# Optimization experiments

Hardware: AMD Instinct MI355X
Metric: run time of the kernel (lower is better)

## Reference

```python
import jax, jax.numpy as jnp
import numpy as np

N_ENT = 100000   # n_entities
N_REL = 64       # n_relations
E_DIM = 64       # e_dim == r_dim (rel2ent is None)
K = 32           # neighbors per entity
B = 1024         # batch of seed entities
SLOPE = 0.2      # LeakyReLU negative_slope


def _xavier(key, shape, fan_in, fan_out):
    b = (6.0 / (fan_in + fan_out)) ** 0.5
    return jax.random.uniform(key, shape, jnp.float32, -b, b)


def setup_inputs() -> dict:
    key = jax.random.key(0)
    ks = jax.random.split(key, 10)
    E = _xavier(ks[0], (N_ENT, E_DIM), N_ENT, E_DIM)          # entity_embs.weight
    R = _xavier(ks[1], (N_REL, E_DIM), N_REL, E_DIM)          # relation_embs.weight
    att_w1 = _xavier(ks[2], (E_DIM, 2 * E_DIM), 2 * E_DIM, E_DIM)  # attention[0], no bias
    att_w2 = _xavier(ks[3], (E_DIM, E_DIM), E_DIM, E_DIM)          # attention[2], no bias
    att_w3 = _xavier(ks[4], (1, E_DIM), E_DIM, 1)                  # attention[4], no bias
    wx_w = _xavier(ks[5], (E_DIM, E_DIM), E_DIM, E_DIM)            # Wx[0].weight
    wx_b = jnp.zeros((E_DIM,), jnp.float32)                        # Wx[0].bias
    wc_w = _xavier(ks[6], (E_DIM, 2 * E_DIM), 2 * E_DIM, E_DIM)    # W_concat.weight
    wc_b = jnp.zeros((E_DIM,), jnp.float32)                        # W_concat.bias
    entity_idx = jax.random.randint(ks[7], (B,), 0, N_ENT)
    adj_entity = jax.random.randint(ks[8], (N_ENT, K), 0, N_ENT)
    adj_relation = jax.random.randint(ks[9], (N_ENT, K), 0, N_REL)
    return {
        "entity_idx": entity_idx, "adj_entity": adj_entity, "adj_relation": adj_relation,
        "E": E, "R": R, "att_w1": att_w1, "att_w2": att_w2, "att_w3": att_w3,
        "wx_w": wx_w, "wx_b": wx_b, "wc_w": wc_w, "wc_b": wc_b,
    }


def _lookup(W, idx):
    # nn.Embedding(max_norm=1): rows whose L2 norm exceeds 1 are renormalized.
    e = W[idx]
    n = jnp.linalg.norm(e, axis=-1, keepdims=True)
    return e * jnp.where(n > 1.0, 1.0 / (n + 1e-7), 1.0)


def _forward(entity_idx, adj_entity, adj_relation, E, R,
             att_w1, att_w2, att_w3, wx_w, wx_b, wc_w, wc_b):
    leaky = lambda x: jnp.where(x >= 0, x, SLOPE * x)
    # attention MLP on cat([h, r]): split first linear so the broadcast h term
    # is computed once per batch row instead of materializing [B, N, 2e].
    w1h, w1r = att_w1[:, :E_DIM], att_w1[:, E_DIM:]

    def gat(h, r, t):
        # h: [B, e] (broadcast over neighbors), r,t: [B, N, e]
        hid = jax.nn.relu(jnp.einsum('be,fe->bf', h, w1h)[:, None, :]
                          + jnp.einsum('bne,fe->bnf', r, w1r))
        hid = jax.nn.relu(jnp.einsum('bnf,gf->bng', hid, att_w2))
        a = jax.nn.sigmoid(jnp.einsum('bng,og->bno', hid, att_w3)[..., 0])  # [B, N]
        w = jax.nn.softmax(a, axis=-1)
        agg = jnp.einsum('bn,bne->be', w, t)       # softmax-weighted neighbor sum
        return agg @ wx_w.T + wx_b                 # per-head Linear (n_heads=1)

    Bsz = entity_idx.shape[0]
    # hop-1 / hop-2 neighbor index gathers (get_neighbors)
    ent1 = adj_entity[entity_idx]                  # [B, K]
    rel1 = adj_relation[entity_idx]                # [B, K]
    ent2 = adj_entity[ent1].reshape(Bsz, -1)       # [B, K*K]
    rel2 = adj_relation[ent1].reshape(Bsz, -1)     # [B, K*K]

    h = _lookup(E, entity_idx)                     # [B, e]
    t1 = _lookup(E, ent1)                          # [B, K, e]
    t2 = _lookup(E, ent2)                          # [B, K*K, e]
    r1 = _lookup(R, rel1)
    r2 = _lookup(R, rel2)

    # iter 0: seed entity broadcast as head
    v1 = leaky(gat(h, r1, t1))                                      # [B, e]
    emb1 = leaky(jnp.concatenate([h, v1], -1) @ wc_w.T + wc_b)      # aggregate 'concat'
    # iter 1: summed hop-1 neighborhood as head
    hsum = t1.sum(axis=1)                                           # [B, e]
    v2 = leaky(gat(hsum, r2, t2))
    emb2 = leaky(jnp.concatenate([hsum, v2], -1) @ wc_w.T + wc_b)
    # sum_aggregator 'concat': e_u = cat(embs[2], cat(embs[1], embs[0]))
    return jnp.concatenate([emb2, emb1, h], axis=-1)                # [B, 3e]


def reference(entity_idx, adj_entity, adj_relation, E, R,
              att_w1, att_w2, att_w3, wx_w, wx_b, wc_w, wc_b):
    return _forward(entity_idx, adj_entity, adj_relation, E, R,
                    att_w1, att_w2, att_w3, wx_w, wx_b, wc_w, wc_b)
```

## Files before the change

kernel.cpp:

```cpp
#include <hip/hip_runtime.h>

#define SLOPE 0.2f

__device__ __forceinline__ float leaky(float x) { return x >= 0.f ? x : SLOPE * x; }

enum : int {
  OFF_PT   = 0,
  OFF_W2T  = OFF_PT + 4096,
  OFF_A3   = OFF_W2T + 4096,
  OFF_WXT  = OFF_A3 + 64,
  OFF_WXB  = OFF_WXT + 4096,
  OFF_WCT  = OFF_WXB + 64,
  OFF_WCB  = OFF_WCT + 8192,
  OFF_W1HT = OFF_WCB + 64,
  WS_FLOATS = OFF_W1HT + 4096
};

__global__ __launch_bounds__(256) void k1_prep(
    const float* __restrict__ R, const float* __restrict__ w1,
    const float* __restrict__ w2, const float* __restrict__ w3,
    const float* __restrict__ wxw, const float* __restrict__ wxb,
    const float* __restrict__ wcw, const float* __restrict__ wcb,
    float* __restrict__ ws) {
  __shared__ float Rn[64 * 65];
  int tid = threadIdx.x, wv = tid >> 6, lane = tid & 63;
  for (int r = wv; r < 64; r += 4) {
    float v = R[r * 64 + lane];
    float ss = v * v;
    #pragma unroll
    for (int m = 1; m < 64; m <<= 1) ss += __shfl_xor(ss, m, 64);
    float n = sqrtf(ss);
    float sc = n > 1.f ? 1.f / (n + 1e-7f) : 1.f;
    Rn[r * 65 + lane] = v * sc;
  }
  __syncthreads();
  int gt = blockIdx.x * 256 + tid;
  for (int i = gt; i < 4096; i += 2048) {
    int f = i >> 6, r = i & 63;
    float acc = 0.f;
    #pragma unroll
    for (int e = 0; e < 64; ++e) acc += Rn[r * 65 + e] * w1[f * 128 + 64 + e];
    ws[OFF_PT + f * 64 + r] = acc;
  }
  for (int i = gt; i < 4096; i += 2048) {
    int f = i >> 6, g = i & 63;
    ws[OFF_W2T + i] = w2[g * 64 + f];
  }
  for (int i = gt; i < 4096; i += 2048) {
    int e = i >> 6, f = i & 63;
    ws[OFF_WXT + i]  = wxw[f * 64 + e];
    ws[OFF_W1HT + i] = w1[f * 128 + e];
  }
  for (int i = gt; i < 8192; i += 2048) {
    int e = i >> 6, f = i & 63;
    ws[OFF_WCT + i] = wcw[f * 128 + e];
  }
  if (gt < 64) {
    ws[OFF_A3 + gt]  = w3[gt];
    ws[OFF_WXB + gt] = wxb[gt];
    ws[OFF_WCB + gt] = wcb[gt];
  }
}

__global__ __launch_bounds__(512, 8) void k_main(
    const int* __restrict__ entity_idx, const int* __restrict__ adj_entity,
    const int* __restrict__ adj_relation, const float* __restrict__ E,
    const float* __restrict__ ws, float* __restrict__ out) {
  __shared__ float s_t1[32 * 64];
  __shared__ float s_partA[8][64], s_partB[8][64];
  __shared__ int   s_ent1[32], s_rel1[32];
  __shared__ int   s_ei[1024];
  __shared__ float s_w[1024];
  __shared__ float s_h[64], s_hs[64], s_hq1[64], s_hq2[64];
  __shared__ float s_at1[64], s_at2[64], s_agg1[64], s_agg2[64], s_v1[64], s_v2[64];
  __shared__ float s_L1, s_L2;
  int b = blockIdx.x, tid = threadIdx.x, wv = tid >> 6, lane = tid & 63;
  int sub = lane >> 4, eg = lane & 15;
  const float4* E4 = (const float4*)E;
  int idx = entity_idx[b];

  if (tid < 64) s_h[tid] = E[(long)idx * 64 + tid];
  if (tid >= 64 && tid < 96) {
    int i = tid - 64;
    s_ent1[i] = adj_entity[(long)idx * 32 + i];
    s_rel1[i] = adj_relation[(long)idx * 32 + i];
  }
  if (tid == 0) s_L2 = 0.f;
  __syncthreads();

  {
    float hs = 0.f;
    #pragma unroll
    for (int k = 0; k < 4; ++k) {
      int n = wv * 4 + k;
      float v = E[(long)s_ent1[n] * 64 + lane];
      s_t1[n * 64 + lane] = v;
      hs += v;
    }
    s_partA[wv][lane] = hs;
  }
  __syncthreads();
  if (tid < 64) {
    float t = 0.f;
    #pragma unroll
    for (int w = 0; w < 8; ++w) t += s_partA[w][tid];
    s_hs[tid] = t;
  }
  __syncthreads();

  {
    const float* src = (wv < 4) ? s_h : s_hs;
    int e0 = (wv & 3) * 16;
    float p = 0.f;
    #pragma unroll
    for (int e = 0; e < 16; ++e) p += ws[OFF_W1HT + (e0 + e) * 64 + lane] * src[e0 + e];
    s_partB[wv][lane] = p;
  }
  __syncthreads();
  if (tid < 64) {
    s_hq1[tid] = s_partB[0][tid] + s_partB[1][tid] + s_partB[2][tid] + s_partB[3][tid];
  } else if (tid < 128) {
    int i = tid - 64;
    s_hq2[i] = s_partB[4][i] + s_partB[5][i] + s_partB[6][i] + s_partB[7][i];
  }
  __syncthreads();

  {
    int swv = __builtin_amdgcn_readfirstlane(wv);
    const float* W2T = ws + OFF_W2T;
    const float* A3  = ws + OFF_A3;
    const float* PT  = ws + OFF_PT;
    float acc1[8], acc2[8];
    #pragma unroll
    for (int i = 0; i < 8; ++i) { acc1[i] = 0.f; acc2[i] = 0.f; }
    int g0 = swv * 8;
    #pragma unroll 2
    for (int f = 0; f < 64; ++f) {
      float ptv = PT[f * 64 + lane];
      float h1 = fmaxf(s_hq1[f] + ptv, 0.f);
      float h2 = fmaxf(s_hq2[f] + ptv, 0.f);
      const float* w = W2T + f * 64 + g0;
      #pragma unroll
      for (int i = 0; i < 8; ++i) { acc1[i] += w[i] * h1; acc2[i] += w[i] * h2; }
    }
    float s1 = 0.f, s2 = 0.f;
    #pragma unroll
    for (int i = 0; i < 8; ++i) {
      float a3 = A3[g0 + i];
      s1 += a3 * fmaxf(acc1[i], 0.f);
      s2 += a3 * fmaxf(acc2[i], 0.f);
    }
    s_partA[wv][lane] = s1;
    s_partB[wv][lane] = s2;
  }
  __syncthreads();
  if (tid < 64) {
    float t = 0.f;
    #pragma unroll
    for (int w = 0; w < 8; ++w) t += s_partA[w][tid];
    float a = 1.f / (1.f + __expf(-t));
    s_at1[tid] = __expf(a);
  } else if (tid < 128) {
    int i = tid - 64;
    float t = 0.f;
    #pragma unroll
    for (int w = 0; w < 8; ++w) t += s_partB[w][i];
    float a = 1.f / (1.f + __expf(-t));
    s_at2[i] = __expf(a);
  }
  __syncthreads();

  {
    float wsum = 0.f;
    #pragma unroll
    for (int i = 0; i < 2; ++i) {
      int n = tid + i * 512;
      int j = n >> 5, i2 = n & 31;
      long base = (long)s_ent1[j] * 32 + i2;
      int ei = adj_entity[base];
      int ri = adj_relation[base];
      float wgt = s_at2[ri];
      s_ei[n] = ei;
      s_w[n] = wgt;
      wsum += wgt;
    }
    #pragma unroll
    for (int m = 1; m < 64; m <<= 1) wsum += __shfl_xor(wsum, m, 64);
    if (lane == 0) atomicAdd(&s_L2, wsum);
  }
  if (tid < 32) {
    float w = s_at1[s_rel1[tid]];
    #pragma unroll
    for (int m = 1; m < 32; m <<= 1) w += __shfl_xor(w, m, 64);
    if (tid == 0) s_L1 = w;
  }
  __syncthreads();

  {
    float4 acc = {0.f, 0.f, 0.f, 0.f};
    for (int t = 0; t < 8; ++t) {
      float4 v[4];
      int nb = t * 4 * 32 + wv * 4 + sub;
      #pragma unroll
      for (int j = 0; j < 4; ++j)
        v[j] = E4[(long)s_ei[nb + j * 32] * 16 + eg];
      #pragma unroll
      for (int j = 0; j < 4; ++j) {
        float wgt = s_w[nb + j * 32];
        acc.x += wgt * v[j].x; acc.y += wgt * v[j].y;
        acc.z += wgt * v[j].z; acc.w += wgt * v[j].w;
      }
    }
    #pragma unroll
    for (int m = 16; m < 64; m <<= 1) {
      acc.x += __shfl_xor(acc.x, m, 64); acc.y += __shfl_xor(acc.y, m, 64);
      acc.z += __shfl_xor(acc.z, m, 64); acc.w += __shfl_xor(acc.w, m, 64);
    }
    if (sub == 0) {
      s_partB[wv][eg * 4 + 0] = acc.x; s_partB[wv][eg * 4 + 1] = acc.y;
      s_partB[wv][eg * 4 + 2] = acc.z; s_partB[wv][eg * 4 + 3] = acc.w;
    }
  }
  {
    float a1 = 0.f;
    #pragma unroll
    for (int k = 0; k < 4; ++k) {
      int n = wv * 4 + k;
      a1 += s_at1[s_rel1[n]] * s_t1[n * 64 + lane];
    }
    s_partA[wv][lane] = a1;
  }
  __syncthreads();
  if (tid < 64) {
    float a = 0.f;
    #pragma unroll
    for (int w = 0; w < 8; ++w) a += s_partA[w][tid];
    s_agg1[tid] = a / s_L1;
  } else if (tid < 128) {
    int i = tid - 64;
    float a = 0.f;
    #pragma unroll
    for (int w = 0; w < 8; ++w) a += s_partB[w][i];
    s_agg2[i] = a / s_L2;
  }
  __syncthreads();

  {
    const float* src = (wv < 4) ? s_agg1 : s_agg2;
    int e0 = (wv & 3) * 16;
    float p = 0.f;
    #pragma unroll
    for (int e = 0; e < 16; ++e)
      p += ws[OFF_WXT + (e0 + e) * 64 + lane] * src[e0 + e];
    s_partA[wv][lane] = p;
  }
  __syncthreads();
  if (tid < 64) {
    float p = s_partA[0][tid] + s_partA[1][tid] + s_partA[2][tid] + s_partA[3][tid];
    s_v1[tid] = leaky(ws[OFF_WXB + tid] + p);
  } else if (tid < 128) {
    int i = tid - 64;
    float p = s_partA[4][i] + s_partA[5][i] + s_partA[6][i] + s_partA[7][i];
    s_v2[i] = leaky(ws[OFF_WXB + i] + p);
  }
  __syncthreads();

  {
    int half = wv >> 2, q = wv & 3;
    const float* src = (q < 2) ? (half ? s_hs : s_h) : (half ? s_v2 : s_v1);
    int e0 = q * 32;
    int o0 = (q & 1) * 32;
    float p = 0.f;
    #pragma unroll 8
    for (int e = 0; e < 32; ++e)
      p += ws[OFF_WCT + (e0 + e) * 64 + lane] * src[o0 + e];
    s_partB[wv][lane] = p;
  }
  __syncthreads();
  if (tid < 64) {
    float o = ws[OFF_WCB + tid] + s_partB[0][tid] + s_partB[1][tid]
            + s_partB[2][tid] + s_partB[3][tid];
    out[b * 192 + 64 + tid]  = leaky(o);
    out[b * 192 + 128 + tid] = s_h[tid];
  } else if (tid < 128) {
    int i = tid - 64;
    float o = ws[OFF_WCB + i] + s_partB[4][i] + s_partB[5][i]
            + s_partB[6][i] + s_partB[7][i];
    out[b * 192 + i] = leaky(o);
  }
}

extern "C" void kernel_launch(void* const* d_in, const int* in_sizes, int n_in,
                              void* d_out, int out_size, void* d_ws, size_t ws_size,
                              hipStream_t stream) {
  const int* entity_idx   = (const int*)d_in[0];
  const int* adj_entity   = (const int*)d_in[1];
  const int* adj_relation = (const int*)d_in[2];
  const float* E          = (const float*)d_in[3];
  const float* R          = (const float*)d_in[4];
  const float* att_w1     = (const float*)d_in[5];
  const float* att_w2     = (const float*)d_in[6];
  const float* att_w3     = (const float*)d_in[7];
  const float* wx_w       = (const float*)d_in[8];
  const float* wx_b       = (const float*)d_in[9];
  const float* wc_w       = (const float*)d_in[10];
  const float* wc_b       = (const float*)d_in[11];
  float* out              = (float*)d_out;
  float* ws               = (float*)d_ws;

  hipLaunchKernelGGL(k1_prep, dim3(8), dim3(256), 0, stream,
                     R, att_w1, att_w2, att_w3, wx_w, wx_b, wc_w, wc_b, ws);
  hipLaunchKernelGGL(k_main, dim3(1024), dim3(512), 0, stream,
                     entity_idx, adj_entity, adj_relation, E, ws, out);
}
```

Measured before the change: 165.8 us.

## Convert entity table to bf16 each call and gather hop-2 rows in bf16

The prep kernel gains 1600 extra blocks that convert the whole 100000x64 fp32 entity table into packed bf16 with round-to-nearest-even and write it to workspace. The hop-2 weighted aggregation then gathers 128-byte bf16 rows as uint4 instead of 256-byte fp32 rows, unpacks them to fp32 and accumulates with a new lane mapping. The aim is to halve the random-gather bytes for the 1024 neighbour rows per seed. The trade is a full-table conversion pass on every call (about 25.6MB read and 12.8MB written) plus reduced precision in that aggregation.

```diff
diff --git a/kernel.cpp b/kernel.cpp
--- a/kernel.cpp
+++ b/kernel.cpp
@@ -13,7 +13,8 @@
   OFF_WCT  = OFF_WXB + 64,
   OFF_WCB  = OFF_WCT + 8192,
   OFF_W1HT = OFF_WCB + 64,
-  WS_FLOATS = OFF_W1HT + 4096
+  WS_FLOATS = OFF_W1HT + 4096,
+  EBF_U32  = 3200000
 };
 
 __global__ __launch_bounds__(256) void k1_prep(
@@ -21,9 +22,24 @@
     const float* __restrict__ w2, const float* __restrict__ w3,
     const float* __restrict__ wxw, const float* __restrict__ wxb,
     const float* __restrict__ wcw, const float* __restrict__ wcb,
-    float* __restrict__ ws) {
+    const float* __restrict__ E, float* __restrict__ ws) {
+  int tid = threadIdx.x;
+  if (blockIdx.x >= 8) {
+    const float2* E2 = (const float2*)E;
+    unsigned* Ebf = (unsigned*)ws + WS_FLOATS;
+    int stride = (gridDim.x - 8) * 256;
+    for (int i = (blockIdx.x - 8) * 256 + tid; i < EBF_U32; i += stride) {
+      float2 f = E2[i];
+      unsigned ua = __float_as_uint(f.x);
+      ua += 0x7FFFu + ((ua >> 16) & 1u);
+      unsigned ub = __float_as_uint(f.y);
+      ub += 0x7FFFu + ((ub >> 16) & 1u);
+      Ebf[i] = (ua >> 16) | (ub & 0xFFFF0000u);
+    }
+    return;
+  }
   __shared__ float Rn[64 * 65];
-  int tid = threadIdx.x, wv = tid >> 6, lane = tid & 63;
+  int wv = tid >> 6, lane = tid & 63;
   for (int r = wv; r < 64; r += 4) {
     float v = R[r * 64 + lane];
     float ss = v * v;
@@ -75,8 +91,8 @@
   __shared__ float s_at1[64], s_at2[64], s_agg1[64], s_agg2[64], s_v1[64], s_v2[64];
   __shared__ float s_L1, s_L2;
   int b = blockIdx.x, tid = threadIdx.x, wv = tid >> 6, lane = tid & 63;
-  int sub = lane >> 4, eg = lane & 15;
   const float4* E4 = (const float4*)E;
+  (void)E4;
   int idx = entity_idx[b];
 
   if (tid < 64) s_h[tid] = E[(long)idx * 64 + tid];
@@ -197,28 +213,41 @@
   __syncthreads();
 
   {
-    float4 acc = {0.f, 0.f, 0.f, 0.f};
-    for (int t = 0; t < 8; ++t) {
-      float4 v[4];
-      int nb = t * 4 * 32 + wv * 4 + sub;
-      #pragma unroll
-      for (int j = 0; j < 4; ++j)
-        v[j] = E4[(long)s_ei[nb + j * 32] * 16 + eg];
+    const uint4* Ebf = (const uint4*)((const unsigned*)ws + WS_FLOATS);
+    int sub8 = lane >> 3, eg8 = lane & 7;
+    float acc[8];
+    #pragma unroll
+    for (int k = 0; k < 8; ++k) acc[k] = 0.f;
+    for (int t = 0; t < 4; ++t) {
+      uint4 v[4];
+      float wgt[4];
       #pragma unroll
       for (int j = 0; j < 4; ++j) {
-        float wgt = s_w[nb + j * 32];
-        acc.x += wgt * v[j].x; acc.y += wgt * v[j].y;
-        acc.z += wgt * v[j].z; acc.w += wgt * v[j].w;
+        int n = (t * 4 + j) * 64 + wv * 8 + sub8;
+        v[j] = Ebf[(long)s_ei[n] * 8 + eg8];
+        wgt[j] = s_w[n];
       }
-    }
-    #pragma unroll
-    for (int m = 16; m < 64; m <<= 1) {
-      acc.x += __shfl_xor(acc.x, m, 64); acc.y += __shfl_xor(acc.y, m, 64);
-      acc.z += __shfl_xor(acc.z, m, 64); acc.w += __shfl_xor(acc.w, m, 64);
-    }
-    if (sub == 0) {
-      s_partB[wv][eg * 4 + 0] = acc.x; s_partB[wv][eg * 4 + 1] = acc.y;
-      s_partB[wv][eg * 4 + 2] = acc.z; s_partB[wv][eg * 4 + 3] = acc.w;
+      #pragma unroll
+      for (int j = 0; j < 4; ++j) {
+        float w = wgt[j];
+        acc[0] += w * __uint_as_float(v[j].x << 16);
+        acc[1] += w * __uint_as_float(v[j].x & 0xFFFF0000u);
+        acc[2] += w * __uint_as_float(v[j].y << 16);
+        acc[3] += w * __uint_as_float(v[j].y & 0xFFFF0000u);
+        acc[4] += w * __uint_as_float(v[j].z << 16);
+        acc[5] += w * __uint_as_float(v[j].z & 0xFFFF0000u);
+        acc[6] += w * __uint_as_float(v[j].w << 16);
+        acc[7] += w * __uint_as_float(v[j].w & 0xFFFF0000u);
+      }
+    }
+    #pragma unroll
+    for (int m = 8; m < 64; m <<= 1) {
+      #pragma unroll
+      for (int k = 0; k < 8; ++k) acc[k] += __shfl_xor(acc[k], m, 64);
+    }
+    if (sub8 == 0) {
+      #pragma unroll
+      for (int k = 0; k < 8; ++k) s_partB[wv][eg8 * 8 + k] = acc[k];
     }
   }
   {
@@ -308,8 +337,8 @@
   float* out              = (float*)d_out;
   float* ws               = (float*)d_ws;
 
-  hipLaunchKernelGGL(k1_prep, dim3(8), dim3(256), 0, stream,
-                     R, att_w1, att_w2, att_w3, wx_w, wx_b, wc_w, wc_b, ws);
+  hipLaunchKernelGGL(k1_prep, dim3(1608), dim3(256), 0, stream,
+                     R, att_w1, att_w2, att_w3, wx_w, wx_b, wc_w, wc_b, E, ws);
   hipLaunchKernelGGL(k_main, dim3(1024), dim3(512), 0, stream,
                      entity_idx, adj_entity, adj_relation, E, ws, out);
 }
```

New measurement: 192.4 us. 16.0% more time.
